# Performance work log

Measured on AMD Instinct MI355X. Metric: run time of the kernel, lower is better.

Reference implementation:

```python
import jax, jax.numpy as jnp
import numpy as np

B, C, H, W = 8, 256, 48, 48
QC = C // 8                # query/key channels
MIP = max(8, C // 32)      # CoordAtt bottleneck channels
EPS = 1e-5                 # BatchNorm eps (inference, running_mean=0, running_var=1)


def _conv1x1(x, Wt, b=None):
    # 1x1 conv == channel matmul: x [b,c,h,w], Wt [o,c]
    y = jnp.einsum('bchw,oc->bohw', x, Wt)
    if b is not None:
        y = y + b[None, :, None, None]
    return y


def _bn(x, w, b):
    # inference BatchNorm with running_mean=0, running_var=1
    s = w * np.float32(1.0 / np.sqrt(1.0 + EPS))
    return x * s[None, :, None, None] + b[None, :, None, None]


def setup_inputs() -> dict:
    key = jax.random.key(0)
    ks = jax.random.split(key, 22)
    r = lambda k, sh, s=0.05: jax.random.normal(k, sh, jnp.float32) * s
    return dict(
        f1=jax.random.normal(ks[0], (B, C, H, W), jnp.float32),
        f2=jax.random.normal(ks[1], (B, C, H, W), jnp.float32),
        t1=r(ks[2], (1, C, 1, 1), 1.0),
        t2=r(ks[3], (1, C, 1, 1), 1.0),
        Wq=r(ks[4], (QC, C)), bq=r(ks[5], (QC,)),
        Wk=r(ks[6], (QC, C)), bk=r(ks[7], (QC,)),
        Wv=r(ks[8], (C, C)), bv=r(ks[9], (C,)),
        gamma=jnp.full((1,), 0.5, jnp.float32),
        ca_w1=r(ks[10], (MIP, C)), ca_b1=r(ks[11], (MIP,)),
        ca_bn_w=1.0 + r(ks[12], (MIP,)), ca_bn_b=r(ks[13], (MIP,)),
        ca_wh=r(ks[14], (C, MIP)), ca_bh=r(ks[15], (C,)),
        ca_ww=r(ks[16], (C, MIP)), ca_bw=r(ks[17], (C,)),
        fus_w=r(ks[18], (C, 2 * C)),
        fus_bn_w=1.0 + r(ks[19], (C,)), fus_bn_b=r(ks[20], (C,)),
    )


def _cross_attention(f1, f2, t1, t2, Wq, bq, Wk, bk, Wv, bv, gamma):
    b, c, h, w = f1.shape
    N = h * w
    f1e = f1 + t1
    f2e = f2 + t2

    def qkv(fe):
        q = _conv1x1(fe, Wq, bq).reshape(b, QC, N).transpose(0, 2, 1)  # [b,N,qc]
        k = _conv1x1(fe, Wk, bk).reshape(b, QC, N)                     # [b,qc,N]
        v = _conv1x1(fe, Wv, bv).reshape(b, c, N)                      # [b,c,N]
        return q, k, v

    q1, k1, v1 = qkv(f1e)
    q2, k2, v2 = qkv(f2e)

    # CrossAtt_1 = softmax(Q2 @ K1^T) applied to V1
    attn21 = jax.nn.softmax(jnp.einsum('bmq,bqn->bmn', q2, k1), axis=-1)  # [b,N,N]
    out1 = jnp.einsum('bcn,bmn->bcm', v1, attn21).reshape(b, c, h, w)
    # CrossAtt_2 = softmax(Q1 @ K2^T) applied to V2
    attn12 = jax.nn.softmax(jnp.einsum('bmq,bqn->bmn', q1, k2), axis=-1)
    out2 = jnp.einsum('bcn,bmn->bcm', v2, attn12).reshape(b, c, h, w)

    return gamma[0] * out1 + f1, gamma[0] * out2 + f2


def _coord_att(x, w1, b1, bnw, bnb, wh, bh, ww, bw):
    b, c, h, w = x.shape
    x_h = jnp.mean(x, axis=3, keepdims=True)                         # [b,c,h,1]
    x_w = jnp.mean(x, axis=2, keepdims=True).transpose(0, 1, 3, 2)   # [b,c,w,1]
    y = jnp.concatenate([x_h, x_w], axis=2)                          # [b,c,h+w,1]
    y = jax.nn.relu(_bn(_conv1x1(y, w1, b1), bnw, bnb))
    yh, yw = y[:, :, :h], y[:, :, h:]
    a_h = jax.nn.sigmoid(_conv1x1(yh, wh, bh))                       # [b,c,h,1]
    a_w = jax.nn.sigmoid(_conv1x1(yw.transpose(0, 1, 3, 2), ww, bw)) # [b,c,1,w]
    return x * a_w * a_h


def _fusion(x, Wf, bnw, bnb):
    return jax.nn.relu(_bn(_conv1x1(x, Wf), bnw, bnb))


def reference(f1, f2, t1, t2, Wq, bq, Wk, bk, Wv, bv, gamma,
              ca_w1, ca_b1, ca_bn_w, ca_bn_b, ca_wh, ca_bh, ca_ww, ca_bw,
              fus_w, fus_bn_w, fus_bn_b):
    a1, a2 = _cross_attention(f1, f2, t1, t2, Wq, bq, Wk, bk, Wv, bv, gamma)
    c1 = _coord_att(f1, ca_w1, ca_b1, ca_bn_w, ca_bn_b, ca_wh, ca_bh, ca_ww, ca_bw)
    c2 = _coord_att(f2, ca_w1, ca_b1, ca_bn_w, ca_bn_b, ca_wh, ca_bh, ca_ww, ca_bw)
    o1 = _fusion(jnp.concatenate([a1, c1], axis=1), fus_w, fus_bn_w, fus_bn_b)
    o2 = _fusion(jnp.concatenate([a2, c2], axis=1), fus_w, fus_bn_w, fus_bn_b)
    return o1, o2
```

## Files before the change

kernel.cpp:

```cpp
#include <hip/hip_runtime.h>
#include <hip/hip_bf16.h>

typedef unsigned short ushort_t;
typedef __attribute__((ext_vector_type(8))) short short8;
typedef __attribute__((ext_vector_type(4))) float floatx4;
typedef __attribute__((ext_vector_type(16))) float floatx16;
typedef __attribute__((ext_vector_type(4))) unsigned int uintx4;


__device__ __forceinline__ float bf2f(ushort_t u) {
    return __uint_as_float(((unsigned int)u) << 16);
}
__device__ __forceinline__ ushort_t f2bf(float f) {
    unsigned int x = __float_as_uint(f);
    unsigned int r = (x + 0x7fffu + ((x >> 16) & 1u)) >> 16;
    return (ushort_t)r;
}
__device__ __forceinline__ unsigned int pkbf(float a, float b) {
    __hip_bfloat162 h = __float22bfloat162_rn(float2{a, b});
    return *reinterpret_cast<unsigned int*>(&h);
}
__device__ __forceinline__ float loadIn(const void* p, size_t i, int isbf) {
    return isbf ? bf2f(((const ushort_t*)p)[i]) : ((const float*)p)[i];
}
__device__ __forceinline__ float fexp2(float x) {
#if __has_builtin(__builtin_amdgcn_exp2f)
    return __builtin_amdgcn_exp2f(x);
#else
    return exp2f(x);
#endif
}
__device__ __forceinline__ void plswap(unsigned& a, unsigned& b, int h) {
#if __has_builtin(__builtin_amdgcn_permlane32_swap)
    auto r = __builtin_amdgcn_permlane32_swap(a, b, false, false);
    a = r[0];
    b = r[1];
#else
    unsigned sa = __shfl_xor(a, 32), sb = __shfl_xor(b, 32);
    unsigned na = (h == 0) ? a : sb;
    unsigned nb = (h == 0) ? sa : b;
    a = na; b = nb;
#endif
}

#define BN_SCALE 0.9999950000374997f
#define LOG2E    1.4426950408889634f
#define ZERO16 (floatx16){0.f,0.f,0.f,0.f,0.f,0.f,0.f,0.f,0.f,0.f,0.f,0.f,0.f,0.f,0.f,0.f}

#define P_T1    0
#define P_T2    256
#define P_WQ    512
#define P_BQ    8704
#define P_WK    8768
#define P_BK    16960
#define P_WV    17024
#define P_BV    82560
#define P_GAMMA 82624
#define P_CAW1  82688
#define P_CAB1  84736
#define P_BNW   84800
#define P_BNB   84864
#define P_WH    84928
#define P_BH    86976
#define P_WW    87232
#define P_BW    89280
#define P_FUSW  89536
#define P_FBNW  220608
#define P_FBNB  220864
#define P_BQ2   221120

__global__ void detect_kernel(const void* gamma, int* flag) {
    if (threadIdx.x == 0) {
        ushort_t u = ((const ushort_t*)gamma)[0];
        *flag = (u != 0) ? 1 : 0;
    }
}

__global__ __launch_bounds__(256) void convert_params(
    const void* t1, const void* t2, const void* Wq, const void* bq,
    const void* Wk, const void* bk, const void* Wv, const void* bv,
    const void* gm, const void* cw1, const void* cb1, const void* bnw,
    const void* bnb, const void* wh, const void* bh, const void* ww,
    const void* bw, const void* fw, const void* fbnw, const void* fbnb,
    const int* flagp, float* dst, ushort_t* WA, ushort_t* WF)
{
    int isbf = *flagp;
    const void* srcs[20] = {t1,t2,Wq,bq,Wk,bk,Wv,bv,gm,cw1,cb1,bnw,bnb,wh,bh,ww,bw,fw,fbnw,fbnb};
    const int   cnts[20] = {256,256,8192,32,8192,32,65536,256,1,2048,8,8,8,2048,256,2048,256,131072,256,256};
    const int   offs[20] = {P_T1,P_T2,P_WQ,P_BQ,P_WK,P_BK,P_WV,P_BV,P_GAMMA,P_CAW1,P_CAB1,
                            P_BNW,P_BNB,P_WH,P_BH,P_WW,P_BW,P_FUSW,P_FBNW,P_FBNB};
    int tid = blockIdx.x * 256 + threadIdx.x;
    int stride = gridDim.x * 256;
    #pragma unroll
    for (int sg = 0; sg < 20; sg++) {
        float* d = dst + offs[sg];
        for (int i = tid; i < cnts[sg]; i += stride) d[i] = loadIn(srcs[sg], i, isbf);
    }
    for (int i = tid; i < 81920; i += stride) {
        int o = i >> 8, c = i & 255;
        float v;
        if (o < 32)      v = loadIn(Wq, o * 256 + c, isbf);
        else if (o < 64) v = loadIn(Wk, (o - 32) * 256 + c, isbf);
        else             v = loadIn(Wv, (size_t)(o - 64) * 256 + c, isbf);
        WA[i] = f2bf(v);
    }
    for (int i = tid; i < 131072; i += stride) WF[i] = f2bf(loadIn(fw, i, isbf));
    int gw = tid >> 6, lane = tid & 63;
    if (gw < 640) {
        int side = gw / 320, o = gw % 320;
        const void* tsrc = side ? t2 : t1;
        float bias; const void* Wsrc; size_t wbase;
        if (o < 32)      { bias = loadIn(bq, o, isbf);       Wsrc = Wq; wbase = (size_t)o * 256; }
        else if (o < 64) { bias = loadIn(bk, o - 32, isbf);  Wsrc = Wk; wbase = (size_t)(o - 32) * 256; }
        else             { bias = loadIn(bv, o - 64, isbf);  Wsrc = Wv; wbase = (size_t)(o - 64) * 256; }
        float s = 0.f;
        for (int c = lane; c < 256; c += 64) s += loadIn(Wsrc, wbase + c, isbf) * loadIn(tsrc, c, isbf);
        s += __shfl_xor(s, 1);  s += __shfl_xor(s, 2);  s += __shfl_xor(s, 4);
        s += __shfl_xor(s, 8);  s += __shfl_xor(s, 16); s += __shfl_xor(s, 32);
        if (lane == 0) dst[P_BQ2 + gw] = bias + s;
    }
}

__global__ __launch_bounds__(256) void prep1_kernel(
    const void* __restrict__ f1, const void* __restrict__ f2,
    const int* __restrict__ flagp, ushort_t* __restrict__ fT)
{
    __shared__ ushort_t tr[64][264];
    int isbf = *flagp;
    int blk = blockIdx.x;
    int nt = blk % 36, sb = blk / 36;
    int side = sb >> 3, b = sb & 7;
    int n0 = nt * 64;
    const void* f = side ? f2 : f1;
    int t = threadIdx.x;
    size_t base = ((size_t)b * 256 + t) * 2304 + n0;
    if (isbf) {
        const ushort_t* fp = (const ushort_t*)f + base;
        #pragma unroll
        for (int i = 0; i < 8; i++) {
            uint4 raw = *(const uint4*)&fp[i * 8];
            const ushort_t* rp = (const ushort_t*)&raw;
            #pragma unroll
            for (int j = 0; j < 8; j++) tr[i * 8 + j][t] = rp[j];
        }
    } else {
        const float* fp = (const float*)f + base;
        #pragma unroll
        for (int i = 0; i < 16; i++) {
            float4 raw = *(const float4*)&fp[i * 4];
            unsigned u0 = pkbf(raw.x, raw.y), u1 = pkbf(raw.z, raw.w);
            tr[i * 4 + 0][t] = (ushort_t)u0;
            tr[i * 4 + 1][t] = (ushort_t)(u0 >> 16);
            tr[i * 4 + 2][t] = (ushort_t)u1;
            tr[i * 4 + 3][t] = (ushort_t)(u1 >> 16);
        }
    }
    __syncthreads();
    #pragma unroll
    for (int i = 0; i < 8; i++) {
        int chunk = i * 256 + t;
        int row = chunk >> 5, k8 = (chunk & 31) * 8;
        *(uint4*)&fT[((size_t)sb * 2304 + n0 + row) * 256 + k8] = *(const uint4*)&tr[row][k8];
    }
}

__global__ __launch_bounds__(256) void qkv_gemm(
    const ushort_t* __restrict__ fT, const ushort_t* __restrict__ WA,
    const float* __restrict__ P,
    ushort_t* __restrict__ qG, ushort_t* __restrict__ kG, ushort_t* __restrict__ vG)
{
    __shared__ ushort_t xs[64][264];
    int blk = blockIdx.x;
    int nt = blk % 36, sb = blk / 36;
    int side = sb >> 3;
    int n0 = nt * 64;
    int t = threadIdx.x;
    int w = t >> 6, l = t & 63, q = l >> 4, ln = l & 15;
    #pragma unroll
    for (int i = 0; i < 8; i++) {
        int chunk = i * 256 + t;
        int row = chunk >> 5, k8 = (chunk & 31) * 8;
        *(uint4*)&xs[row][k8] = *(const uint4*)&fT[((size_t)sb * 2304 + n0 + row) * 256 + k8];
    }
    __syncthreads();
    floatx4 acc[5][4];
    #pragma unroll
    for (int mi = 0; mi < 5; mi++)
        #pragma unroll
        for (int ns = 0; ns < 4; ns++) acc[mi][ns] = (floatx4){0.f, 0.f, 0.f, 0.f};
    #pragma unroll
    for (int ks = 0; ks < 8; ks++) {
        short8 a[5];
        #pragma unroll
        for (int mi = 0; mi < 5; mi++)
            a[mi] = *(const short8*)&WA[(size_t)(w * 80 + mi * 16 + ln) * 256 + ks * 32 + q * 8];
        #pragma unroll
        for (int ns = 0; ns < 4; ns++) {
            short8 bfr = *(const short8*)&xs[ns * 16 + ln][ks * 32 + q * 8];
            #pragma unroll
            for (int mi = 0; mi < 5; mi++)
                acc[mi][ns] = __builtin_amdgcn_mfma_f32_16x16x32_bf16(a[mi], bfr, acc[mi][ns], 0, 0, 0);
        }
    }
    const float* bp = P + P_BQ2 + side * 320;
    #pragma unroll
    for (int mi = 0; mi < 5; mi++) {
        int o0 = w * 80 + mi * 16 + q * 4;
        #pragma unroll
        for (int ns = 0; ns < 4; ns++) {
            int n = n0 + ns * 16 + ln;
            if (o0 < 32) {
                uint2 pk;
                pk.x = pkbf((acc[mi][ns][0] + bp[o0]) * LOG2E, (acc[mi][ns][1] + bp[o0 + 1]) * LOG2E);
                pk.y = pkbf((acc[mi][ns][2] + bp[o0 + 2]) * LOG2E, (acc[mi][ns][3] + bp[o0 + 3]) * LOG2E);
                *(uint2*)&qG[((size_t)sb * 2304 + n) * 32 + o0] = pk;
            } else if (o0 < 64) {
                uint2 pk;
                pk.x = pkbf(acc[mi][ns][0] + bp[o0], acc[mi][ns][1] + bp[o0 + 1]);
                pk.y = pkbf(acc[mi][ns][2] + bp[o0 + 2], acc[mi][ns][3] + bp[o0 + 3]);
                *(uint2*)&kG[((size_t)sb * 2304 + n) * 32 + (o0 - 32)] = pk;
            } else {
                unsigned u0 = pkbf(acc[mi][ns][0] + bp[o0], acc[mi][ns][1] + bp[o0 + 1]);
                unsigned u1 = pkbf(acc[mi][ns][2] + bp[o0 + 2], acc[mi][ns][3] + bp[o0 + 3]);
                vG[((size_t)sb * 256 + (o0 - 64 + 0)) * 2304 + n] = (ushort_t)u0;
                vG[((size_t)sb * 256 + (o0 - 64 + 1)) * 2304 + n] = (ushort_t)(u0 >> 16);
                vG[((size_t)sb * 256 + (o0 - 64 + 2)) * 2304 + n] = (ushort_t)u1;
                vG[((size_t)sb * 256 + (o0 - 64 + 3)) * 2304 + n] = (ushort_t)(u1 >> 16);
            }
        }
    }
}

__global__ __launch_bounds__(256) void pool_kernel(
    const ushort_t* __restrict__ fT, float* __restrict__ pools)
{
    int blk = blockIdx.x;
    int j = blk % 96, sb = blk / 96;
    int c = threadIdx.x;
    const ushort_t* base = fT + (size_t)sb * 2304 * 256 + c;
    float s = 0.f;
    if (j < 48) {
        int h = j;
        #pragma unroll 8
        for (int w = 0; w < 48; w++) s += bf2f(base[(size_t)(h * 48 + w) * 256]);
    } else {
        int w = j - 48;
        #pragma unroll 8
        for (int h = 0; h < 48; h++) s += bf2f(base[(size_t)(h * 48 + w) * 256]);
    }
    pools[(size_t)sb * 24576 + c * 96 + j] = s * (1.f / 48.f);
}

__global__ __launch_bounds__(256) void coord_kernel(
    const float* __restrict__ pools, const float* __restrict__ P,
    float* __restrict__ attv)
{
    __shared__ float w1s[8][256];
    __shared__ float ys[8][96];
    int sb = blockIdx.x;
    int t = threadIdx.x;
    for (int ff = t; ff < 2048; ff += 256) w1s[ff >> 8][ff & 255] = P[P_CAW1 + ff];
    __syncthreads();
    const float* pin = pools + (size_t)sb * 24576;
    if (t < 96) {
        float s[8];
        #pragma unroll
        for (int mp = 0; mp < 8; mp++) s[mp] = 0.f;
        for (int c = 0; c < 256; c++) {
            float p = pin[c * 96 + t];
            #pragma unroll
            for (int mp = 0; mp < 8; mp++) s[mp] += w1s[mp][c] * p;
        }
        #pragma unroll
        for (int mp = 0; mp < 8; mp++) {
            float vv = s[mp] + P[P_CAB1 + mp];
            vv = vv * (P[P_BNW + mp] * BN_SCALE) + P[P_BNB + mp];
            ys[mp][t] = fmaxf(vv, 0.f);
        }
    }
    __syncthreads();
    float* aout = attv + (size_t)sb * 24576;
    for (int ff = t; ff < 24576; ff += 256) {
        int j = ff >> 8, c = ff & 255;
        const float* W = P + ((j < 48) ? P_WH : P_WW);
        const float* B = P + ((j < 48) ? P_BH : P_BW);
        float s = B[c];
        #pragma unroll
        for (int mp = 0; mp < 8; mp++) s += W[c * 8 + mp] * ys[mp][j];
        aout[ff] = 1.f / (1.f + __expf(-s));
    }
}

__global__ __launch_bounds__(256) void attn_kernel(
    const ushort_t* __restrict__ qG, const ushort_t* __restrict__ kG,
    const ushort_t* __restrict__ vG,
    ushort_t* __restrict__ O0, ushort_t* __restrict__ O1,
    float* __restrict__ lbuf)
{
    __shared__ __align__(16) ushort_t vsm[4][64 * 68];
    __shared__ __align__(16) ushort_t paf[8192];
    __shared__ float lred[4][32];

    int i = blockIdx.x;
    int xcd = i & 7, slot = i >> 3;
    int dhi = (slot >= 72) ? 1 : 0;
    int db = xcd + (dhi << 3);
    int rem = slot - 72 * dhi;
    int sp = rem & 1, mt = rem >> 1;
    int qsb = db ^ 8;

    int t = threadIdx.x;
    int w = t >> 6;
    int qsw = w & 1, ksw = w >> 1;
    int l = t & 63, r31 = l & 31, h = l >> 5;
    int q0 = mt * 64, c0 = w * 64;

    short8 qf0, qf1;
    {
        const ushort_t* qrow = qG + ((size_t)qsb * 2304 + q0 + qsw * 32 + r31) * 32;
        qf0 = *(const short8*)&qrow[h * 8];
        qf1 = *(const short8*)&qrow[16 + h * 8];
    }

    const ushort_t* kW = kG + ((size_t)db * 2304 + ksw * 32 + r31) * 32 + h * 8;
    const ushort_t* vbase = vG + ((size_t)db * 256 + c0) * 2304;
    ushort_t* vw = &vsm[w][0];
    int vls = (l >> 3);
    int vlc = (l & 7) * 8;

    floatx16 o[2][2];
    #pragma unroll
    for (int qs = 0; qs < 2; qs++)
        #pragma unroll
        for (int cs = 0; cs < 2; cs++) o[qs][cs] = ZERO16;
    float l_lane = 0.f;

    int nstart = sp * 1152;

#define V_LOAD(VR, N0)                                                         \
    _Pragma("unroll")                                                          \
    for (int i_ = 0; i_ < 8; i_++) {                                           \
        int r_ = i_ * 8 + vls;                                                 \
        VR[i_] = *(const uint4*)&vbase[(size_t)r_ * 2304 + (N0) + vlc];        \
    }
#define V_STORE(VR)                                                            \
    _Pragma("unroll")                                                          \
    for (int i_ = 0; i_ < 8; i_++) {                                           \
        int a_ = (i_ * 8 + vls) * 68 + vlc;                                    \
        *(uint2*)&vw[a_]     = make_uint2(VR[i_].x, VR[i_].y);                 \
        *(uint2*)&vw[a_ + 4] = make_uint2(VR[i_].z, VR[i_].w);                 \
    }

#define DO_S_PUBLISH(K0, K1, BUF)                                              \
    {                                                                          \
        floatx16 s_ = ZERO16;                                                  \
        s_ = __builtin_amdgcn_mfma_f32_32x32x16_bf16(K0, qf0, s_, 0, 0, 0);    \
        s_ = __builtin_amdgcn_mfma_f32_32x32x16_bf16(K1, qf1, s_, 0, 0, 0);    \
        float e_[16];                                                          \
        _Pragma("unroll")                                                      \
        for (int r_ = 0; r_ < 16; r_++) e_[r_] = fexp2(s_[r_]);                \
        l_lane += (((e_[0] + e_[1]) + (e_[2] + e_[3]))                         \
                 + ((e_[4] + e_[5]) + (e_[6] + e_[7])))                        \
                + (((e_[8] + e_[9]) + (e_[10] + e_[11]))                       \
                 + ((e_[12] + e_[13]) + (e_[14] + e_[15])));                   \
        unsigned wd_[8];                                                       \
        _Pragma("unroll")                                                      \
        for (int p_ = 0; p_ < 8; p_++) wd_[p_] = pkbf(e_[2 * p_], e_[2 * p_ + 1]); \
        plswap(wd_[0], wd_[2], h); plswap(wd_[1], wd_[3], h);                  \
        plswap(wd_[4], wd_[6], h); plswap(wd_[5], wd_[7], h);                  \
        uintx4 A0_ = {wd_[0], wd_[1], wd_[2], wd_[3]};                         \
        uintx4 A1_ = {wd_[4], wd_[5], wd_[6], wd_[7]};                         \
        *(uintx4*)&paf[(size_t)((((BUF) * 2 + qsw) * 4 + ksw * 2 + 0) * 64 + l) * 8] = A0_; \
        *(uintx4*)&paf[(size_t)((((BUF) * 2 + qsw) * 4 + ksw * 2 + 1) * 64 + l) * 8] = A1_; \
    }

#define DO_PV(BUF)                                                             \
    __builtin_amdgcn_s_setprio(1);                                             \
    _Pragma("unroll")                                                          \
    for (int kt = 0; kt < 4; kt++) {                                           \
        short8 af0 = *(const short8*)&paf[(size_t)((((BUF) * 2 + 0) * 4 + kt) * 64 + l) * 8]; \
        short8 af1 = *(const short8*)&paf[(size_t)((((BUF) * 2 + 1) * 4 + kt) * 64 + l) * 8]; \
        _Pragma("unroll")                                                      \
        for (int cs = 0; cs < 2; cs++) {                                       \
            int va_ = (cs * 32 + r31) * 68 + kt * 16 + h * 8;                  \
            uint2 u0_ = *(const uint2*)&vw[va_];                               \
            uint2 u1_ = *(const uint2*)&vw[va_ + 4];                           \
            uintx4 vv_ = {u0_.x, u0_.y, u1_.x, u1_.y};                         \
            short8 vf_ = *(const short8*)&vv_;                                 \
            o[0][cs] = __builtin_amdgcn_mfma_f32_32x32x16_bf16(af0, vf_, o[0][cs], 0, 0, 0); \
            o[1][cs] = __builtin_amdgcn_mfma_f32_32x32x16_bf16(af1, vf_, o[1][cs], 0, 0, 0); \
        }                                                                      \
    }                                                                          \
    __builtin_amdgcn_s_setprio(0);

    uint4 vr[8];
    V_LOAD(vr, nstart)
    {
        const ushort_t* kp = kW + (size_t)nstart * 32;
        short8 k0 = *(const short8*)&kp[0];
        short8 k1 = *(const short8*)&kp[16];
        DO_S_PUBLISH(k0, k1, 0)
    }
    V_STORE(vr)
    __syncthreads();

    for (int tile = 0; tile < 17; tile++) {
        int n0 = nstart + tile * 64;
        int buf = tile & 1;
        const ushort_t* kp = kW + (size_t)(n0 + 64) * 32;
        short8 k0n = *(const short8*)&kp[0];
        short8 k1n = *(const short8*)&kp[16];
        V_LOAD(vr, n0 + 64)
        DO_PV(buf)
        DO_S_PUBLISH(k0n, k1n, (buf ^ 1))
        V_STORE(vr)
        __syncthreads();
    }
    DO_PV(1)
#undef DO_PV
#undef DO_S_PUBLISH
#undef V_STORE
#undef V_LOAD

    float lt = l_lane + __shfl_xor(l_lane, 32);
    lred[w][r31] = lt;
    ushort_t* Op = sp ? O1 : O0;
    size_t obase = ((size_t)db * 2304 + q0) * 256 + c0;
    ushort_t* ow = vw;
    int rrow8 = l >> 3, rch0 = (l & 7) * 8;
    #pragma unroll
    for (int qs = 0; qs < 2; qs++) {
        #pragma unroll
        for (int cs = 0; cs < 2; cs++) {
            #pragma unroll
            for (int r = 0; r < 16; r++) {
                int qloc = (r & 3) + 8 * (r >> 2) + 4 * h;
                ow[qloc * 72 + cs * 32 + r31] = f2bf(o[qs][cs][r]);
            }
        }
        #pragma unroll
        for (int pass = 0; pass < 4; pass++) {
            int row = pass * 8 + rrow8;
            uintx4 v = *(const uintx4*)&ow[row * 72 + rch0];
            __builtin_nontemporal_store(v, (uintx4*)&Op[obase + (size_t)(qs * 32 + row) * 256 + rch0]);
        }
    }
    __syncthreads();
    if (t < 64) {
        int base = ((db * 36 + mt) * 2 + sp) * 64;
        int qs = t >> 5, r = t & 31;
        lbuf[base + t] = lred[qs][r] + lred[qs + 2][r];
    }
}

__global__ __launch_bounds__(256) void fusion_gemm(
    const ushort_t* __restrict__ O0, const ushort_t* __restrict__ O1,
    const ushort_t* __restrict__ fT, const float* __restrict__ attv,
    const float* __restrict__ lbuf,
    const ushort_t* __restrict__ WF, const float* __restrict__ P,
    const int* __restrict__ flagp, void* __restrict__ dout)
{
    __shared__ ushort_t xs[64][264];
    __shared__ float sS[64];
    int isbf = *flagp;
    int blk = blockIdx.x;
    int nt = blk % 36, sb = blk / 36;
    int n0 = nt * 64;
    int t = threadIdx.x;
    int w = t >> 6, l = t & 63, q = l >> 4, ln = l & 15;
    if (t < 64) {
        float l0 = lbuf[(sb * 36 + nt) * 128 + t];
        float l1 = lbuf[(sb * 36 + nt) * 128 + 64 + t];
        sS[t] = P[P_GAMMA] / (l0 + l1);
    }
    __syncthreads();
    floatx4 acc[4][4];
    #pragma unroll
    for (int ms = 0; ms < 4; ms++)
        #pragma unroll
        for (int ns = 0; ns < 4; ns++) acc[ms][ns] = (floatx4){0.f, 0.f, 0.f, 0.f};
    size_t tbase = ((size_t)sb * 2304 + n0) * 256;
    #pragma unroll
    for (int i = 0; i < 8; i++) {
        int chunk = i * 256 + t;
        int row = chunk >> 5, k8 = (chunk & 31) * 8;
        size_t idx = tbase + (size_t)row * 256 + k8;
        uintx4 u0 = __builtin_nontemporal_load((const uintx4*)&O0[idx]);
        uintx4 u1 = __builtin_nontemporal_load((const uintx4*)&O1[idx]);
        uint4 uf = *(const uint4*)&fT[idx];
        const ushort_t* a0 = (const ushort_t*)&u0;
        const ushort_t* a1 = (const ushort_t*)&u1;
        const ushort_t* ff = (const ushort_t*)&uf;
        float s = sS[row];
        float v[8];
        #pragma unroll
        for (int j = 0; j < 8; j++) v[j] = (bf2f(a0[j]) + bf2f(a1[j])) * s + bf2f(ff[j]);
        uint4 pk;
        pk.x = pkbf(v[0], v[1]); pk.y = pkbf(v[2], v[3]);
        pk.z = pkbf(v[4], v[5]); pk.w = pkbf(v[6], v[7]);
        *(uint4*)&xs[row][k8] = pk;
    }
    __syncthreads();
    #pragma unroll
    for (int ks = 0; ks < 8; ks++) {
        short8 a[4];
        #pragma unroll
        for (int ms = 0; ms < 4; ms++)
            a[ms] = *(const short8*)&WF[(size_t)(w * 64 + ms * 16 + ln) * 512 + ks * 32 + q * 8];
        #pragma unroll
        for (int ns = 0; ns < 4; ns++) {
            short8 bfr = *(const short8*)&xs[ns * 16 + ln][ks * 32 + q * 8];
            #pragma unroll
            for (int ms = 0; ms < 4; ms++)
                acc[ms][ns] = __builtin_amdgcn_mfma_f32_16x16x32_bf16(a[ms], bfr, acc[ms][ns], 0, 0, 0);
        }
    }
    __syncthreads();
    const float* av = attv + (size_t)sb * 24576;
    #pragma unroll
    for (int i = 0; i < 8; i++) {
        int chunk = i * 256 + t;
        int row = chunk >> 5, k8 = (chunk & 31) * 8;
        int n = n0 + row;
        int h = n / 48, ww2 = n - h * 48;
        size_t idx = tbase + (size_t)row * 256 + k8;
        uint4 uf = *(const uint4*)&fT[idx];
        const ushort_t* ff = (const ushort_t*)&uf;
        float ah[8], aw[8];
        *(float4*)&ah[0] = *(const float4*)&av[h * 256 + k8];
        *(float4*)&ah[4] = *(const float4*)&av[h * 256 + k8 + 4];
        *(float4*)&aw[0] = *(const float4*)&av[(48 + ww2) * 256 + k8];
        *(float4*)&aw[4] = *(const float4*)&av[(48 + ww2) * 256 + k8 + 4];
        float v[8];
        #pragma unroll
        for (int j = 0; j < 8; j++) v[j] = bf2f(ff[j]) * ah[j] * aw[j];
        uint4 pk;
        pk.x = pkbf(v[0], v[1]); pk.y = pkbf(v[2], v[3]);
        pk.z = pkbf(v[4], v[5]); pk.w = pkbf(v[6], v[7]);
        *(uint4*)&xs[row][k8] = pk;
    }
    __syncthreads();
    #pragma unroll
    for (int ks = 0; ks < 8; ks++) {
        short8 a[4];
        #pragma unroll
        for (int ms = 0; ms < 4; ms++)
            a[ms] = *(const short8*)&WF[(size_t)(w * 64 + ms * 16 + ln) * 512 + 256 + ks * 32 + q * 8];
        #pragma unroll
        for (int ns = 0; ns < 4; ns++) {
            short8 bfr = *(const short8*)&xs[ns * 16 + ln][ks * 32 + q * 8];
            #pragma unroll
            for (int ms = 0; ms < 4; ms++)
                acc[ms][ns] = __builtin_amdgcn_mfma_f32_16x16x32_bf16(a[ms], bfr, acc[ms][ns], 0, 0, 0);
        }
    }
    #pragma unroll
    for (int ms = 0; ms < 4; ms++) {
        int o0 = w * 64 + ms * 16 + q * 4;
        float bw[4], bb[4];
        #pragma unroll
        for (int r = 0; r < 4; r++) {
            bw[r] = P[P_FBNW + o0 + r] * BN_SCALE;
            bb[r] = P[P_FBNB + o0 + r];
        }
        #pragma unroll
        for (int ns = 0; ns < 4; ns++) {
            int n = n0 + ns * 16 + ln;
            #pragma unroll
            for (int r = 0; r < 4; r++) {
                float v = acc[ms][ns][r] * bw[r] + bb[r];
                v = (v < 0.f) ? 0.f : v;
                size_t oidx = (size_t)sb * 589824 + (size_t)(o0 + r) * 2304 + n;
                if (isbf) ((ushort_t*)dout)[oidx] = f2bf(v);
                else      ((float*)dout)[oidx] = v;
            }
        }
    }
}

extern "C" void kernel_launch(void* const* d_in, const int* in_sizes, int n_in,
                              void* d_out, int out_size, void* d_ws, size_t ws_size,
                              hipStream_t stream) {
    const void* f1 = d_in[0]; const void* f2 = d_in[1];

    char* ws = (char*)d_ws;
    int*      flag  = (int*)(ws + 0);
    float*    P     = (float*)(ws + 1024);
    ushort_t* WA    = (ushort_t*)(ws + 917504);
    ushort_t* WF    = (ushort_t*)(ws + 1081344);
    ushort_t* fT    = (ushort_t*)(ws + 1343488);
    ushort_t* qG    = (ushort_t*)(ws + 20217856);
    ushort_t* kG    = (ushort_t*)(ws + 22577152);
    ushort_t* vG    = (ushort_t*)(ws + 24936448);
    ushort_t* O0    = (ushort_t*)(ws + 43810816);
    float*    pools = (float*)(ws + 62685184);
    float*    attv  = (float*)(ws + 64258048);
    ushort_t* O1    = (ushort_t*)(ws + 65830912);
    float*    lbuf  = pools;

    detect_kernel<<<dim3(1), dim3(64), 0, stream>>>(d_in[10], flag);
    convert_params<<<dim3(160), dim3(256), 0, stream>>>(
        d_in[2], d_in[3], d_in[4], d_in[5], d_in[6], d_in[7], d_in[8], d_in[9],
        d_in[10], d_in[11], d_in[12], d_in[13], d_in[14], d_in[15], d_in[16],
        d_in[17], d_in[18], d_in[19], d_in[20], d_in[21], flag, P, WA, WF);
    prep1_kernel<<<dim3(576), dim3(256), 0, stream>>>(f1, f2, flag, fT);
    qkv_gemm<<<dim3(576), dim3(256), 0, stream>>>(fT, WA, P, qG, kG, vG);
    pool_kernel<<<dim3(1536), dim3(256), 0, stream>>>(fT, pools);
    coord_kernel<<<dim3(16), dim3(256), 0, stream>>>(pools, P, attv);
    attn_kernel<<<dim3(1152), dim3(256), 0, stream>>>(qG, kG, vG, O0, O1, lbuf);
    fusion_gemm<<<dim3(576), dim3(256), 0, stream>>>(
        O0, O1, fT, attv, lbuf, WF, P, flag, d_out);
}
```

Baseline: 344.5 us.

## Fuse prep with QKV GEMM, merge coord into attention launch, atomic row sums

The transpose/convert kernel and the QKV GEMM become one kernel. The GEMM now reads the bf16 tile straight from shared memory instead of reloading fT from global memory. The coordinate-attention kernel runs as 16 extra blocks of the attention launch, and pool_kernel zeroes a row-sum buffer. Attention blocks then accumulate softmax denominators into that buffer with atomicAdd, replacing the per-block lbuf partials and the final block barrier. This cuts two kernel launches and one global round trip. The row-sum buffer reuses the WA workspace region after WA is consumed, which depends on launch order staying the same.

Result: faster. 319.5 us (-7.2%).

```diff
diff --git a/kernel.cpp b/kernel.cpp
--- a/kernel.cpp
+++ b/kernel.cpp
@@ -69,6 +69,8 @@
 #define P_FBNB  220864
 #define P_BQ2   221120
 
+#define ATTN_BLOCKS 1152
+
 __global__ void detect_kernel(const void* gamma, int* flag) {
     if (threadIdx.x == 0) {
         ushort_t u = ((const ushort_t*)gamma)[0];
@@ -121,11 +123,14 @@
     }
 }
 
-__global__ __launch_bounds__(256) void prep1_kernel(
+__global__ __launch_bounds__(256) void prep_qkv(
     const void* __restrict__ f1, const void* __restrict__ f2,
-    const int* __restrict__ flagp, ushort_t* __restrict__ fT)
+    const int* __restrict__ flagp,
+    const ushort_t* __restrict__ WA, const float* __restrict__ P,
+    ushort_t* __restrict__ fT,
+    ushort_t* __restrict__ qG, ushort_t* __restrict__ kG, ushort_t* __restrict__ vG)
 {
-    __shared__ ushort_t tr[64][264];
+    __shared__ ushort_t xs[64][264];
     int isbf = *flagp;
     int blk = blockIdx.x;
     int nt = blk % 36, sb = blk / 36;
@@ -141,7 +146,7 @@
             uint4 raw = *(const uint4*)&fp[i * 8];
             const ushort_t* rp = (const ushort_t*)&raw;
             #pragma unroll
-            for (int j = 0; j < 8; j++) tr[i * 8 + j][t] = rp[j];
+            for (int j = 0; j < 8; j++) xs[i * 8 + j][t] = rp[j];
         }
     } else {
         const float* fp = (const float*)f + base;
@@ -149,10 +154,10 @@
         for (int i = 0; i < 16; i++) {
             float4 raw = *(const float4*)&fp[i * 4];
             unsigned u0 = pkbf(raw.x, raw.y), u1 = pkbf(raw.z, raw.w);
-            tr[i * 4 + 0][t] = (ushort_t)u0;
-            tr[i * 4 + 1][t] = (ushort_t)(u0 >> 16);
-            tr[i * 4 + 2][t] = (ushort_t)u1;
-            tr[i * 4 + 3][t] = (ushort_t)(u1 >> 16);
+            xs[i * 4 + 0][t] = (ushort_t)u0;
+            xs[i * 4 + 1][t] = (ushort_t)(u0 >> 16);
+            xs[i * 4 + 2][t] = (ushort_t)u1;
+            xs[i * 4 + 3][t] = (ushort_t)(u1 >> 16);
         }
     }
     __syncthreads();
@@ -160,29 +165,9 @@
     for (int i = 0; i < 8; i++) {
         int chunk = i * 256 + t;
         int row = chunk >> 5, k8 = (chunk & 31) * 8;
-        *(uint4*)&fT[((size_t)sb * 2304 + n0 + row) * 256 + k8] = *(const uint4*)&tr[row][k8];
-    }
-}
-
-__global__ __launch_bounds__(256) void qkv_gemm(
-    const ushort_t* __restrict__ fT, const ushort_t* __restrict__ WA,
-    const float* __restrict__ P,
-    ushort_t* __restrict__ qG, ushort_t* __restrict__ kG, ushort_t* __restrict__ vG)
-{
-    __shared__ ushort_t xs[64][264];
-    int blk = blockIdx.x;
-    int nt = blk % 36, sb = blk / 36;
-    int side = sb >> 3;
-    int n0 = nt * 64;
-    int t = threadIdx.x;
+        *(uint4*)&fT[((size_t)sb * 2304 + n0 + row) * 256 + k8] = *(const uint4*)&xs[row][k8];
+    }
     int w = t >> 6, l = t & 63, q = l >> 4, ln = l & 15;
-    #pragma unroll
-    for (int i = 0; i < 8; i++) {
-        int chunk = i * 256 + t;
-        int row = chunk >> 5, k8 = (chunk & 31) * 8;
-        *(uint4*)&xs[row][k8] = *(const uint4*)&fT[((size_t)sb * 2304 + n0 + row) * 256 + k8];
-    }
-    __syncthreads();
     floatx4 acc[5][4];
     #pragma unroll
     for (int mi = 0; mi < 5; mi++)
@@ -232,11 +217,13 @@
 }
 
 __global__ __launch_bounds__(256) void pool_kernel(
-    const ushort_t* __restrict__ fT, float* __restrict__ pools)
+    const ushort_t* __restrict__ fT, float* __restrict__ pools,
+    float* __restrict__ lsum)
 {
     int blk = blockIdx.x;
+    int c = threadIdx.x;
+    if (blk < 576 && c < 64) lsum[blk * 64 + c] = 0.f;
     int j = blk % 96, sb = blk / 96;
-    int c = threadIdx.x;
     const ushort_t* base = fT + (size_t)sb * 2304 * 256 + c;
     float s = 0.f;
     if (j < 48) {
@@ -251,55 +238,55 @@
     pools[(size_t)sb * 24576 + c * 96 + j] = s * (1.f / 48.f);
 }
 
-__global__ __launch_bounds__(256) void coord_kernel(
+__global__ __launch_bounds__(256) void attn_coord(
+    const ushort_t* __restrict__ qG, const ushort_t* __restrict__ kG,
+    const ushort_t* __restrict__ vG,
+    ushort_t* __restrict__ O0, ushort_t* __restrict__ O1,
+    float* __restrict__ lsum,
     const float* __restrict__ pools, const float* __restrict__ P,
     float* __restrict__ attv)
 {
-    __shared__ float w1s[8][256];
-    __shared__ float ys[8][96];
-    int sb = blockIdx.x;
-    int t = threadIdx.x;
-    for (int ff = t; ff < 2048; ff += 256) w1s[ff >> 8][ff & 255] = P[P_CAW1 + ff];
-    __syncthreads();
-    const float* pin = pools + (size_t)sb * 24576;
-    if (t < 96) {
-        float s[8];
-        #pragma unroll
-        for (int mp = 0; mp < 8; mp++) s[mp] = 0.f;
-        for (int c = 0; c < 256; c++) {
-            float p = pin[c * 96 + t];
-            #pragma unroll
-            for (int mp = 0; mp < 8; mp++) s[mp] += w1s[mp][c] * p;
-        }
-        #pragma unroll
-        for (int mp = 0; mp < 8; mp++) {
-            float vv = s[mp] + P[P_CAB1 + mp];
-            vv = vv * (P[P_BNW + mp] * BN_SCALE) + P[P_BNB + mp];
-            ys[mp][t] = fmaxf(vv, 0.f);
-        }
-    }
-    __syncthreads();
-    float* aout = attv + (size_t)sb * 24576;
-    for (int ff = t; ff < 24576; ff += 256) {
-        int j = ff >> 8, c = ff & 255;
-        const float* W = P + ((j < 48) ? P_WH : P_WW);
-        const float* B = P + ((j < 48) ? P_BH : P_BW);
-        float s = B[c];
-        #pragma unroll
-        for (int mp = 0; mp < 8; mp++) s += W[c * 8 + mp] * ys[mp][j];
-        aout[ff] = 1.f / (1.f + __expf(-s));
-    }
-}
-
-__global__ __launch_bounds__(256) void attn_kernel(
-    const ushort_t* __restrict__ qG, const ushort_t* __restrict__ kG,
-    const ushort_t* __restrict__ vG,
-    ushort_t* __restrict__ O0, ushort_t* __restrict__ O1,
-    float* __restrict__ lbuf)
-{
     __shared__ __align__(16) ushort_t vsm[4][64 * 68];
     __shared__ __align__(16) ushort_t paf[8192];
-    __shared__ float lred[4][32];
+
+    int t = threadIdx.x;
+
+    if (blockIdx.x >= ATTN_BLOCKS) {
+        float* w1s = (float*)&vsm[0][0];
+        float* ys  = w1s + 2048;
+        int sb = blockIdx.x - ATTN_BLOCKS;
+        for (int ff = t; ff < 2048; ff += 256) w1s[ff] = P[P_CAW1 + ff];
+        __syncthreads();
+        const float* pin = pools + (size_t)sb * 24576;
+        if (t < 96) {
+            float s[8];
+            #pragma unroll
+            for (int mp = 0; mp < 8; mp++) s[mp] = 0.f;
+            for (int c = 0; c < 256; c++) {
+                float p = pin[c * 96 + t];
+                #pragma unroll
+                for (int mp = 0; mp < 8; mp++) s[mp] += w1s[mp * 256 + c] * p;
+            }
+            #pragma unroll
+            for (int mp = 0; mp < 8; mp++) {
+                float vv = s[mp] + P[P_CAB1 + mp];
+                vv = vv * (P[P_BNW + mp] * BN_SCALE) + P[P_BNB + mp];
+                ys[mp * 96 + t] = fmaxf(vv, 0.f);
+            }
+        }
+        __syncthreads();
+        float* aout = attv + (size_t)sb * 24576;
+        for (int ff = t; ff < 24576; ff += 256) {
+            int j = ff >> 8, c = ff & 255;
+            const float* W = P + ((j < 48) ? P_WH : P_WW);
+            const float* B = P + ((j < 48) ? P_BH : P_BW);
+            float s = B[c];
+            #pragma unroll
+            for (int mp = 0; mp < 8; mp++) s += W[c * 8 + mp] * ys[mp * 96 + j];
+            aout[ff] = 1.f / (1.f + __expf(-s));
+        }
+        return;
+    }
 
     int i = blockIdx.x;
     int xcd = i & 7, slot = i >> 3;
@@ -309,7 +296,6 @@
     int sp = rem & 1, mt = rem >> 1;
     int qsb = db ^ 8;
 
-    int t = threadIdx.x;
     int w = t >> 6;
     int qsw = w & 1, ksw = w >> 1;
     int l = t & 63, r31 = l & 31, h = l >> 5;
@@ -423,7 +409,8 @@
 #undef V_LOAD
 
     float lt = l_lane + __shfl_xor(l_lane, 32);
-    lred[w][r31] = lt;
+    if (h == 0)
+        atomicAdd(&lsum[(size_t)db * 2304 + q0 + qsw * 32 + r31], lt);
     ushort_t* Op = sp ? O1 : O0;
     size_t obase = ((size_t)db * 2304 + q0) * 256 + c0;
     ushort_t* ow = vw;
@@ -445,18 +432,12 @@
             __builtin_nontemporal_store(v, (uintx4*)&Op[obase + (size_t)(qs * 32 + row) * 256 + rch0]);
         }
     }
-    __syncthreads();
-    if (t < 64) {
-        int base = ((db * 36 + mt) * 2 + sp) * 64;
-        int qs = t >> 5, r = t & 31;
-        lbuf[base + t] = lred[qs][r] + lred[qs + 2][r];
-    }
 }
 
 __global__ __launch_bounds__(256) void fusion_gemm(
     const ushort_t* __restrict__ O0, const ushort_t* __restrict__ O1,
     const ushort_t* __restrict__ fT, const float* __restrict__ attv,
-    const float* __restrict__ lbuf,
+    const float* __restrict__ lsum,
     const ushort_t* __restrict__ WF, const float* __restrict__ P,
     const int* __restrict__ flagp, void* __restrict__ dout)
 {
@@ -469,9 +450,7 @@
     int t = threadIdx.x;
     int w = t >> 6, l = t & 63, q = l >> 4, ln = l & 15;
     if (t < 64) {
-        float l0 = lbuf[(sb * 36 + nt) * 128 + t];
-        float l1 = lbuf[(sb * 36 + nt) * 128 + 64 + t];
-        sS[t] = P[P_GAMMA] / (l0 + l1);
+        sS[t] = P[P_GAMMA] / lsum[(size_t)sb * 2304 + n0 + t];
     }
     __syncthreads();
     floatx4 acc[4][4];
@@ -596,18 +575,16 @@
     float*    pools = (float*)(ws + 62685184);
     float*    attv  = (float*)(ws + 64258048);
     ushort_t* O1    = (ushort_t*)(ws + 65830912);
-    float*    lbuf  = pools;
+    float*    lsum  = (float*)(ws + 917504);
 
     detect_kernel<<<dim3(1), dim3(64), 0, stream>>>(d_in[10], flag);
     convert_params<<<dim3(160), dim3(256), 0, stream>>>(
         d_in[2], d_in[3], d_in[4], d_in[5], d_in[6], d_in[7], d_in[8], d_in[9],
         d_in[10], d_in[11], d_in[12], d_in[13], d_in[14], d_in[15], d_in[16],
         d_in[17], d_in[18], d_in[19], d_in[20], d_in[21], flag, P, WA, WF);
-    prep1_kernel<<<dim3(576), dim3(256), 0, stream>>>(f1, f2, flag, fT);
-    qkv_gemm<<<dim3(576), dim3(256), 0, stream>>>(fT, WA, P, qG, kG, vG);
-    pool_kernel<<<dim3(1536), dim3(256), 0, stream>>>(fT, pools);
-    coord_kernel<<<dim3(16), dim3(256), 0, stream>>>(pools, P, attv);
-    attn_kernel<<<dim3(1152), dim3(256), 0, stream>>>(qG, kG, vG, O0, O1, lbuf);
+    prep_qkv<<<dim3(576), dim3(256), 0, stream>>>(f1, f2, flag, WA, P, fT, qG, kG, vG);
+    pool_kernel<<<dim3(1536), dim3(256), 0, stream>>>(fT, pools, lsum);
+    attn_coord<<<dim3(1168), dim3(256), 0, stream>>>(qG, kG, vG, O0, O1, lsum, pools, P, attv);
     fusion_gemm<<<dim3(576), dim3(256), 0, stream>>>(
-        O0, O1, fT, attv, lbuf, WF, P, flag, d_out);
-}
+        O0, O1, fT, attv, lsum, WF, P, flag, d_out);
+}
```
